# Kernel optimization log

Hardware: AMD Instinct MI355X
Metric: run time of the kernel (lower is better)

Reference implementation:

```python
import jax, jax.numpy as jnp
import numpy as np

FILTER_SIZE = 256          # nperseg and conv kernel length
REG = 1e-7
B, C, T = 512, 8, 6000


def welch_psd(x, nperseg):
    # x: [B, C, T]; window=None (rect), fs=1, noverlap=nperseg//2, detrend by segment mean
    noverlap = nperseg // 2
    step = nperseg - noverlap
    num_seg = (x.shape[-1] - noverlap) // step
    idx = jnp.arange(nperseg)[None, :] + step * jnp.arange(num_seg)[:, None]  # [S, nperseg]
    seg = x[..., idx]                                   # [B, C, S, nperseg]
    seg = seg - seg.mean(axis=-1, keepdims=True)
    fft = jnp.fft.rfft(seg, axis=-1)                    # [B, C, S, F]
    psd = jnp.abs(fft) ** 2 / float(nperseg)
    # one-sided scaling: double all bins except DC (and Nyquist for even nperseg)
    if nperseg % 2 == 0:
        psd = psd.at[..., 1:-1].multiply(2.0)
    else:
        psd = psd.at[..., 1:].multiply(2.0)
    return psd.mean(axis=-2)                            # [B, C, F]


def setup_inputs() -> dict:
    key = jax.random.key(0)
    x = jax.random.normal(key, (B, C, T), dtype=jnp.float32)
    return {"x": x}


def reference(x):
    K = FILTER_SIZE
    n_chan = x.shape[1]
    # center
    x = x - x.mean(axis=-1, keepdims=True)
    psd = welch_psd(x, K) + REG                         # [B, C, F]
    F = psd.shape[-1]
    # barycenter (training, first_iter=True): weights = 1/F elementwise, sum over batch, squared; detached
    new_bary = jnp.sum(jnp.sqrt(psd) / F, axis=0) ** 2  # [C, F]
    target = jax.lax.stop_gradient(new_bary)
    # whitening/mapping filter in frequency domain
    D = jnp.sqrt(target)[None] / jnp.sqrt(psd)          # [B, C, F]
    H = jnp.fft.irfft(D, n=K, axis=-1)                  # [B, C, K]
    H = jnp.fft.fftshift(H, axes=-1)
    H = jnp.flip(H, axis=-1)
    # per-sample depthwise conv1d, padding='same' (torch: left=(K-1)//2, right=K//2 for stride 1)
    lp = (K - 1) // 2
    rp = (K - 1) - lp
    def dw(xb, hb):  # xb: [C, T], hb: [C, K]
        return jax.lax.conv_general_dilated(
            xb[None], hb[:, None, :], (1,), [(lp, rp)],
            feature_group_count=n_chan,
            dimension_numbers=("NCH", "OIH", "NCH"))[0]
    return jax.vmap(dw)(x, H)                           # [B, C, T]
```

## Files before the change

### kernel.cpp

```cpp
#include <hip/hip_runtime.h>
#include <math.h>

#define T_LEN 6000
#define NROWS 4096
#define NCH 8
#define F_BINS 129
#define CF (NCH*F_BINS)
#define NSLOT 16
#define REG_EPS 1e-7f

typedef _Float16 half8 __attribute__((ext_vector_type(8)));
typedef _Float16 half4_t __attribute__((ext_vector_type(4)));
typedef float f32x4 __attribute__((ext_vector_type(4)));

#define PSD_ROWS 8
__global__ __launch_bounds__(512, 2) void psd_kernel(const float* __restrict__ x,
                                                     float* __restrict__ psd,
                                                     float* __restrict__ means,
                                                     float* __restrict__ ssum16) {
  int tid = threadIdx.x;
  int lane = tid & 63;
  int w = tid >> 6;
  int l15 = lane & 15, l4 = lane >> 4;
  __shared__ __align__(16) _Float16 xh[2][6272];
  __shared__ float colsum[256];
  __shared__ float rowm[3][8];

  half8 bf[2][8];
  #pragma unroll
  for (int i = 0; i < 2; ++i) {
    int n = 16 * (2 * w + i) + l15;
    int nn = (n < 129) ? n : (n - 128);
    for (int kk = 0; kk < 8; ++kk) {
      half8 hb;
      for (int e = 0; e < 8; ++e) {
        int k = 32 * kk + 8 * l4 + e;
        float ang = (float)((nn * k) & 255) * (6.283185307179586f / 256.f);
        float s, c;
        __sincosf(ang, &s, &c);
        hb[e] = (_Float16)((n < 129) ? c : s);
      }
      bf[i][kk] = hb;
    }
  }

  int r0 = blockIdx.x * PSD_ROWS;
  float* myslot = ssum16 + (size_t)(blockIdx.x & (NSLOT - 1)) * CF;
  float4 v[4];
  {
    const float* xr = x + (size_t)r0 * T_LEN;
    #pragma unroll
    for (int j = 0; j < 4; ++j) {
      int c = tid + 512 * j;
      v[j] = (c < 1500) ? ((const float4*)xr)[c] : make_float4(0.f, 0.f, 0.f, 0.f);
    }
    float rs = 0.f;
    #pragma unroll
    for (int j = 0; j < 4; ++j) {
      int c = tid + 512 * j;
      if (c < 1568) {
        float4 q = v[j];
        rs += q.x + q.y + q.z + q.w;
        half4_t h = { (_Float16)q.x, (_Float16)q.y, (_Float16)q.z, (_Float16)q.w };
        int byte = 8 * c;
        byte ^= ((byte >> 8) & 7) << 4;
        *(half4_t*)((char*)xh[0] + byte) = h;
      }
    }
    #pragma unroll
    for (int off = 32; off >= 1; off >>= 1) rs += __shfl_xor(rs, off);
    if (lane == 0) rowm[0][w] = rs;
    const float* x1 = x + (size_t)(r0 + 1) * T_LEN;
    #pragma unroll
    for (int j = 0; j < 4; ++j) {
      int c = tid + 512 * j;
      v[j] = (c < 1500) ? ((const float4*)x1)[c] : make_float4(0.f, 0.f, 0.f, 0.f);
    }
  }
  __syncthreads();

  for (int jr = 0; jr < PSD_ROWS; ++jr) {
    int r = r0 + jr;
    const char* xcur = (const char*)xh[jr & 1];
    if (jr + 1 < PSD_ROWS) {
      char* xnxt = (char*)xh[(jr + 1) & 1];
      float rs = 0.f;
      #pragma unroll
      for (int j = 0; j < 4; ++j) {
        int c = tid + 512 * j;
        if (c < 1568) {
          float4 q = v[j];
          rs += q.x + q.y + q.z + q.w;
          half4_t h = { (_Float16)q.x, (_Float16)q.y, (_Float16)q.z, (_Float16)q.w };
          int byte = 8 * c;
          byte ^= ((byte >> 8) & 7) << 4;
          *(half4_t*)(xnxt + byte) = h;
        }
      }
      if (jr + 2 < PSD_ROWS) {
        const float* xn = x + (size_t)(r + 2) * T_LEN;
        #pragma unroll
        for (int j = 0; j < 4; ++j) {
          int c = tid + 512 * j;
          v[j] = (c < 1500) ? ((const float4*)xn)[c] : make_float4(0.f, 0.f, 0.f, 0.f);
        }
      }
      #pragma unroll
      for (int off = 32; off >= 1; off >>= 1) rs += __shfl_xor(rs, off);
      if (lane == 0) rowm[(jr + 1) % 3][w] = rs;
    }
    f32x4 acc[2][3];
    #pragma unroll
    for (int i = 0; i < 2; ++i)
      #pragma unroll
      for (int mt = 0; mt < 3; ++mt)
        acc[i][mt] = (f32x4){0.f, 0.f, 0.f, 0.f};
    #pragma unroll
    for (int kk = 0; kk < 8; ++kk) {
      half8 a[3];
      #pragma unroll
      for (int mt = 0; mt < 3; ++mt) {
        int ab = 4096 * mt + 256 * l15 + 64 * kk + 16 * l4;
        ab ^= ((ab >> 8) & 7) << 4;
        a[mt] = *(const half8*)(xcur + ab);
      }
      #pragma unroll
      for (int mt = 0; mt < 3; ++mt) {
        acc[0][mt] = __builtin_amdgcn_mfma_f32_16x16x32_f16(a[mt], bf[0][kk], acc[0][mt], 0, 0, 0);
        acc[1][mt] = __builtin_amdgcn_mfma_f32_16x16x32_f16(a[mt], bf[1][kk], acc[1][mt], 0, 0, 0);
      }
    }
    float s0, s1;
    #pragma unroll
    for (int i = 0; i < 2; ++i) {
      float t = 0.f;
      #pragma unroll
      for (int j = 0; j < 4; ++j) {
        t += acc[i][0][j] * acc[i][0][j];
        t += acc[i][1][j] * acc[i][1][j];
        if (4 * l4 + j < 13) t += acc[i][2][j] * acc[i][2][j];
      }
      t += __shfl_xor(t, 16);
      t += __shfl_xor(t, 32);
      if (i == 0) s0 = t; else s1 = t;
    }
    __syncthreads();
    if (l4 == 0) {
      colsum[16 * (2 * w + 0) + l15] = s0;
      colsum[16 * (2 * w + 1) + l15] = s1;
    }
    __syncthreads();
    if (tid < F_BINS) {
      float vv;
      if (tid == 0) vv = 0.f;
      else if (tid == 128) vv = colsum[128] * (1.f / 11520.f);
      else vv = (colsum[tid] + colsum[tid + 128]) * (1.f / 5760.f);
      float p = vv + REG_EPS;
      psd[(size_t)r * F_BINS + tid] = p;
      atomicAdd(&myslot[jr * F_BINS + tid], sqrtf(p) * (1.f / (float)F_BINS));
    }
    if (tid == 0) {
      float ms = 0.f;
      #pragma unroll
      for (int q = 0; q < 8; ++q) ms += rowm[jr % 3][q];
      means[r] = ms * (1.f / (float)T_LEN);
    }
  }
}

#define BSTRIDE 296
__global__ __launch_bounds__(384) void conv_kernel(const float* __restrict__ x,
                                                   const float* __restrict__ means,
                                                   const float* __restrict__ psd,
                                                   const float* __restrict__ ssum16,
                                                   float* __restrict__ y) {
  int rc = blockIdx.x;
  int c = rc & (NCH - 1);
  int tid = threadIdx.x;
  int lane = tid & 63;
  int w = tid >> 6;
  __shared__ __align__(16) char smem[24576];
  _Float16* xh = (_Float16*)smem;
  _Float16* Bp = (_Float16*)(smem + 13056);
  float* part = (float*)(smem + 13056);
  float* dv = (float*)(smem + 22528);
  float* hv = (float*)(smem + 23044);
  const float* xr = x + (size_t)rc * T_LEN;
  float mean = means[rc];
  if (tid < F_BINS) {
    float s = 0.f;
    #pragma unroll
    for (int p = 0; p < NSLOT; ++p)
      s += ssum16[(size_t)p * CF + c * F_BINS + tid];
    dv[tid] = s * rsqrtf(psd[(size_t)rc * F_BINS + tid]);
  }
  #pragma unroll
  for (int j = 0; j < 5; ++j) {
    int q = tid + 384 * j;
    if (q < 1632) {
      int cc = q - 32;
      half4_t h;
      if (cc >= 0 && cc < 1500) {
        float4 vv = ((const float4*)xr)[cc];
        h = (half4_t){ (_Float16)(vv.x - mean), (_Float16)(vv.y - mean),
                       (_Float16)(vv.z - mean), (_Float16)(vv.w - mean) };
      } else {
        h = (half4_t){ (_Float16)0.f, (_Float16)0.f, (_Float16)0.f, (_Float16)0.f };
      }
      *(half4_t*)((char*)xh + 8 * q) = h;
    }
  }
  __syncthreads();
  if (tid < 258) {
    int t = tid >> 1, p = tid & 1;
    int k0 = p ? 64 : 1;
    int nk = p ? 64 : 63;
    float stc, sts;
    __sincosf((float)t * (6.283185307179586f / 256.f), &sts, &stc);
    float cr, ci;
    __sincosf((float)((t * k0) & 255) * (6.283185307179586f / 256.f), &ci, &cr);
    float acc = 0.f;
    for (int q = 0; q < nk; ++q) {
      acc = fmaf(dv[k0 + q], cr, acc);
      float nr = cr * stc - ci * sts;
      ci = cr * sts + ci * stc;
      cr = nr;
    }
    part[tid] = acc;
  }
  __syncthreads();
  if (tid < F_BINS) {
    float val = dv[0] + ((tid & 1) ? -dv[128] : dv[128]) +
                2.f * (part[2 * tid] + part[2 * tid + 1]);
    hv[tid] = val * (1.f / 256.f);
  }
  __syncthreads();
  #pragma unroll
  for (int j = 0; j < 3; ++j) {
    int idx = tid + 384 * j;
    int n = idx & 15;
    int qq = idx >> 4;
    int s0 = 4 * qq - n - 1;
    half4_t h;
    #pragma unroll
    for (int e = 0; e < 4; ++e) {
      int s = s0 + e;
      float hvv = 0.f;
      if (s >= 0 && s < 256) {
        int ii = s - 127; if (ii < 0) ii = -ii;
        hvv = hv[ii];
      }
      h[e] = (_Float16)hvv;
    }
    *(half4_t*)((char*)Bp + (size_t)n * (2 * BSTRIDE) + 8 * qq) = h;
  }
  __syncthreads();

  int l15 = lane & 15, l4 = lane >> 4;
  f32x4 acc0 = {0.f,0.f,0.f,0.f}, acc1 = {0.f,0.f,0.f,0.f};
  f32x4 acc2 = {0.f,0.f,0.f,0.f}, acc3 = {0.f,0.f,0.f,0.f};
  const _Float16* bbase = &Bp[BSTRIDE * l15 + 8 * l4];
  const _Float16* abase = &xh[16 * l15 + 8 * l4 + 1024 * w];
  #pragma unroll
  for (int kk = 0; kk < 9; ++kk) {
    half8 b = *(const half8*)(bbase + 32 * kk);
    half8 a0 = *(const half8*)(abase + 32 * kk);
    half8 a1 = *(const half8*)(abase + 256 + 32 * kk);
    half8 a2 = *(const half8*)(abase + 512 + 32 * kk);
    half8 a3 = *(const half8*)(abase + 768 + 32 * kk);
    acc0 = __builtin_amdgcn_mfma_f32_16x16x32_f16(a0, b, acc0, 0, 0, 0);
    acc1 = __builtin_amdgcn_mfma_f32_16x16x32_f16(a1, b, acc1, 0, 0, 0);
    acc2 = __builtin_amdgcn_mfma_f32_16x16x32_f16(a2, b, acc2, 0, 0, 0);
    acc3 = __builtin_amdgcn_mfma_f32_16x16x32_f16(a3, b, acc3, 0, 0, 0);
  }
  __syncthreads();
  float* bw = (float*)smem + 1024 * w;
  #pragma unroll
  for (int i = 0; i < 4; ++i) {
    f32x4 a = (i == 0) ? acc0 : (i == 1) ? acc1 : (i == 2) ? acc2 : acc3;
    #pragma unroll
    for (int j = 0; j < 4; ++j)
      bw[256 * i + 64 * l4 + 16 * j + l15] = a[j];
  }
  float* yr = y + (size_t)rc * T_LEN + 1024 * w;
  const float4* b4 = (const float4*)bw;
  #pragma unroll
  for (int cc = 0; cc < 4; ++cc) {
    int fi = 1024 * w + 256 * cc + 4 * lane;
    if (fi < T_LEN)
      *(float4*)&yr[256 * cc + 4 * lane] = b4[64 * cc + lane];
  }
}

extern "C" void kernel_launch(void* const* d_in, const int* in_sizes, int n_in,
                              void* d_out, int out_size, void* d_ws, size_t ws_size,
                              hipStream_t stream) {
  const float* x = (const float*)d_in[0];
  float* out = (float*)d_out;
  float* psd    = (float*)d_ws;
  float* ssum16 = psd + (size_t)NROWS * F_BINS;
  float* means  = ssum16 + (size_t)NSLOT * CF;
  hipMemsetAsync(ssum16, 0, (size_t)NSLOT * CF * sizeof(float), stream);
  psd_kernel<<<NROWS / PSD_ROWS, 512, 0, stream>>>(x, psd, means, ssum16);
  conv_kernel<<<NROWS, 384, 0, stream>>>(x, means, psd, ssum16, out);
}
```

Before: 105.2 us.

## Halve rows per PSD block, double atomic slots, swizzle conv output staging

```diff
diff --git a/kernel.cpp b/kernel.cpp
--- a/kernel.cpp
+++ b/kernel.cpp
@@ -6,18 +6,18 @@
 #define NCH 8
 #define F_BINS 129
 #define CF (NCH*F_BINS)
-#define NSLOT 16
+#define NSLOT 32
 #define REG_EPS 1e-7f
 
 typedef _Float16 half8 __attribute__((ext_vector_type(8)));
 typedef _Float16 half4_t __attribute__((ext_vector_type(4)));
 typedef float f32x4 __attribute__((ext_vector_type(4)));
 
-#define PSD_ROWS 8
+#define PSD_ROWS 4
 __global__ __launch_bounds__(512, 2) void psd_kernel(const float* __restrict__ x,
                                                      float* __restrict__ psd,
                                                      float* __restrict__ means,
-                                                     float* __restrict__ ssum16) {
+                                                     float* __restrict__ ssumN) {
   int tid = threadIdx.x;
   int lane = tid & 63;
   int w = tid >> 6;
@@ -45,7 +45,7 @@
   }
 
   int r0 = blockIdx.x * PSD_ROWS;
-  float* myslot = ssum16 + (size_t)(blockIdx.x & (NSLOT - 1)) * CF;
+  float* myslot = ssumN + (size_t)(blockIdx.x & (NSLOT - 1)) * CF;
   float4 v[4];
   {
     const float* xr = x + (size_t)r0 * T_LEN;
@@ -157,7 +157,7 @@
       else vv = (colsum[tid] + colsum[tid + 128]) * (1.f / 5760.f);
       float p = vv + REG_EPS;
       psd[(size_t)r * F_BINS + tid] = p;
-      atomicAdd(&myslot[jr * F_BINS + tid], sqrtf(p) * (1.f / (float)F_BINS));
+      atomicAdd(&myslot[(r & 7) * F_BINS + tid], sqrtf(p) * (1.f / (float)F_BINS));
     }
     if (tid == 0) {
       float ms = 0.f;
@@ -169,10 +169,11 @@
 }
 
 #define BSTRIDE 296
+#define SWZW(wd) ((wd) ^ ((((wd) >> 6) & 3) << 4))
 __global__ __launch_bounds__(384) void conv_kernel(const float* __restrict__ x,
                                                    const float* __restrict__ means,
                                                    const float* __restrict__ psd,
-                                                   const float* __restrict__ ssum16,
+                                                   const float* __restrict__ ssumN,
                                                    float* __restrict__ y) {
   int rc = blockIdx.x;
   int c = rc & (NCH - 1);
@@ -191,7 +192,7 @@
     float s = 0.f;
     #pragma unroll
     for (int p = 0; p < NSLOT; ++p)
-      s += ssum16[(size_t)p * CF + c * F_BINS + tid];
+      s += ssumN[(size_t)p * CF + c * F_BINS + tid];
     dv[tid] = s * rsqrtf(psd[(size_t)rc * F_BINS + tid]);
   }
   #pragma unroll
@@ -274,21 +275,24 @@
     acc3 = __builtin_amdgcn_mfma_f32_16x16x32_f16(a3, b, acc3, 0, 0, 0);
   }
   __syncthreads();
-  float* bw = (float*)smem + 1024 * w;
+  float* sf = (float*)smem;
   #pragma unroll
   for (int i = 0; i < 4; ++i) {
     f32x4 a = (i == 0) ? acc0 : (i == 1) ? acc1 : (i == 2) ? acc2 : acc3;
     #pragma unroll
-    for (int j = 0; j < 4; ++j)
-      bw[256 * i + 64 * l4 + 16 * j + l15] = a[j];
+    for (int j = 0; j < 4; ++j) {
+      int wd = 1024 * w + 256 * i + 64 * l4 + 16 * j + l15;
+      sf[SWZW(wd)] = a[j];
+    }
   }
   float* yr = y + (size_t)rc * T_LEN + 1024 * w;
-  const float4* b4 = (const float4*)bw;
   #pragma unroll
   for (int cc = 0; cc < 4; ++cc) {
     int fi = 1024 * w + 256 * cc + 4 * lane;
-    if (fi < T_LEN)
-      *(float4*)&yr[256 * cc + 4 * lane] = b4[64 * cc + lane];
+    if (fi < T_LEN) {
+      int wd = 1024 * w + 256 * cc + 4 * lane;
+      *(float4*)&yr[256 * cc + 4 * lane] = *(const float4*)&sf[SWZW(wd)];
+    }
   }
 }
 
@@ -297,10 +301,10 @@
                               hipStream_t stream) {
   const float* x = (const float*)d_in[0];
   float* out = (float*)d_out;
-  float* psd    = (float*)d_ws;
-  float* ssum16 = psd + (size_t)NROWS * F_BINS;
-  float* means  = ssum16 + (size_t)NSLOT * CF;
-  hipMemsetAsync(ssum16, 0, (size_t)NSLOT * CF * sizeof(float), stream);
-  psd_kernel<<<NROWS / PSD_ROWS, 512, 0, stream>>>(x, psd, means, ssum16);
-  conv_kernel<<<NROWS, 384, 0, stream>>>(x, means, psd, ssum16, out);
+  float* psd   = (float*)d_ws;
+  float* ssumN = psd + (size_t)NROWS * F_BINS;
+  float* means = ssumN + (size_t)NSLOT * CF;
+  hipMemsetAsync(ssumN, 0, (size_t)NSLOT * CF * sizeof(float), stream);
+  psd_kernel<<<NROWS / PSD_ROWS, 512, 0, stream>>>(x, psd, means, ssumN);
+  conv_kernel<<<NROWS, 384, 0, stream>>>(x, means, psd, ssumN, out);
 }
```

New measurement: 131.2 us. 1.25x slower.
